# Kernel optimization log

Hardware: AMD Instinct MI355X
Metric: run time of the kernel (lower is better)

The kernel has to match this reference:

```python
import jax, jax.numpy as jnp
import numpy as np

H = 128   # d_model / features
N = 32    # kept complex modes (d_state=64 -> 32 conjugate pairs)
B = 8
L = 8192


def setup_inputs() -> dict:
    key = jax.random.key(0)
    ks = jax.random.split(key, 8)
    x = jax.random.normal(ks[0], (B, H, L), jnp.float32)
    # S4D (diagonal SSM) kernel parameters; channels=2 for bidirectional
    C_re = (jax.random.normal(ks[1], (2, H, N), jnp.float32) * (0.5 ** 0.5))
    C_im = (jax.random.normal(ks[2], (2, H, N), jnp.float32) * (0.5 ** 0.5))
    log_A_real = jnp.log(0.5 * jnp.ones((H, N), jnp.float32))          # S4D-Lin init
    A_imag = jnp.tile(np.pi * jnp.arange(N, dtype=jnp.float32), (H, 1))
    # log_dt uniform in [log(1e-3), log(1e-1)]
    u = jax.random.uniform(ks[3], (H,), jnp.float32)
    log_dt = u * (np.log(0.1) - np.log(0.001)) + np.log(0.001)
    D = jax.random.normal(ks[4], (H,), jnp.float32)                    # skip term
    W_pw = jax.random.normal(ks[5], (H, H), jnp.float32) / np.sqrt(H)  # 1x1 conv weight (out, in)
    gamma = jnp.ones((H,), jnp.float32)
    beta = jnp.zeros((H,), jnp.float32)
    return {"x": x, "C_re": C_re, "C_im": C_im, "log_A_real": log_A_real,
            "A_imag": A_imag, "log_dt": log_dt, "D": D, "W_pw": W_pw,
            "gamma": gamma, "beta": beta}


def reference(x, C_re, C_im, log_A_real, A_imag, log_dt, D, W_pw, gamma, beta):
    Lx = x.shape[-1]
    # ---- S4D SSM kernel via Vandermonde (ZOH discretization) ----
    A = -jnp.exp(log_A_real) + 1j * A_imag                 # (H, N) complex
    dt = jnp.exp(log_dt)[:, None]                          # (H, 1)
    dtA = A * dt                                           # (H, N)
    C = C_re + 1j * C_im                                   # (2, H, N)
    Kc = C * ((jnp.exp(dtA) - 1.0) / A)                    # (2, H, N)
    vand = jnp.exp(dtA[:, :, None] * jnp.arange(Lx))       # (H, N, L)
    k = 2.0 * jnp.einsum('chn,hnl->chl', Kc, vand).real    # (2, H, L)
    # ---- bidirectional: causal half + anticausal (flipped) half ----
    k_full = (jnp.pad(k[0], ((0, 0), (0, Lx)))
              + jnp.pad(k[1][:, ::-1], ((0, 0), (Lx, 0))))  # (H, 2L)
    # ---- FFT convolution ----
    n = 2 * Lx
    y = jnp.fft.irfft(jnp.fft.rfft(x, n=n) * jnp.fft.rfft(k_full, n=n), n=n)[..., :Lx]
    y = y + x * D[:, None]                                 # skip connection
    y = jax.nn.gelu(y, approximate=False)                  # FFTConv default activation
    # ---- pointwise 1x1 conv (no bias) ----
    y = jnp.einsum('bhl,oh->bol', y, W_pw)
    # ---- BatchNorm1d (training-mode batch statistics) ----
    mean = jnp.mean(y, axis=(0, 2), keepdims=True)
    var = jnp.var(y, axis=(0, 2), keepdims=True)
    y = (y - mean) * jax.lax.rsqrt(var + 1e-5) * gamma[:, None] + beta[:, None]
    # ---- ELU + residual (dropout p=0) ----
    return jax.nn.elu(y) + x
```

## Files before the change

kernel.cpp:

```cpp
#include <hip/hip_runtime.h>
#include <math.h>

#define HCH   128
#define NMODE 32
#define BB    8
#define LLEN  8192
#define LC    256
#define CCH   (LLEN / LC)
#define ROWS  (BB * HCH)

typedef unsigned int uint;
typedef _Float16 f16x8 __attribute__((ext_vector_type(8)));
typedef float    f32x4 __attribute__((ext_vector_type(4)));

static __device__ __forceinline__ uint pk2(float a, float b) {
    union { _Float16 h[2]; uint u; } v;
    v.h[0] = (_Float16)a; v.h[1] = (_Float16)b;
    return v.u;
}

__device__ __forceinline__ float gelu_f(float y) {
    float z = fabsf(y) * 0.7071067811865476f;
    float p = fmaf(z, 0.078108f, 0.000972f);
    p = fmaf(z, p, 0.230389f);
    p = fmaf(z, p, 0.278393f);
    p = fmaf(z, p, 1.0f);
    float p2 = p * p;
    float p4 = p2 * p2;
    float er = 1.f - __builtin_amdgcn_rcpf(p4);
    float s  = copysignf(er, y);
    return 0.5f * y * (1.f + s);
}

#define DPP_ADD(v, ctrl) { int _t = __builtin_amdgcn_update_dpp(0, __float_as_int(v), \
                             (ctrl), 0xF, 0xF, true); (v) += __int_as_float(_t); }

__global__ __launch_bounds__(256) void k_prep(const float* __restrict__ C_re,
                                              const float* __restrict__ C_im,
                                              const float* __restrict__ logA,
                                              const float* __restrict__ Aim,
                                              const float* __restrict__ logdt,
                                              const float* __restrict__ W,
                                              _Float16* __restrict__ cT,
                                              uint* __restrict__ kmg,
                                              _Float16* __restrict__ eT,
                                              _Float16* __restrict__ Wh,
                                              float* __restrict__ Pw,
                                              float* __restrict__ stats) {
    __shared__ float2 PL[32 * 257];
    __shared__ float4 G01[32];
    __shared__ float4 HG[32];
    __shared__ float2 WL[32];
    __shared__ float k0L[256], k1L[256];
    __shared__ _Float16 KMl[516];
    int tid  = threadIdx.x;
    int h    = blockIdx.x >> 1;
    int half = blockIdx.x & 1;
    if (blockIdx.x == 0) stats[tid] = 0.f;
    if (half == 0 && tid < 128) Wh[h * 128 + tid] = (_Float16)W[h * 128 + tid];
    if (tid < 32) {
        int n = tid, idx = h * 32 + n;
        float ar = expf(logA[idx]);
        float ai = Aim[idx];
        float dt = expf(logdt[h]);
        float dre = -ar * dt, dim = ai * dt;
        float er = expf(dre);
        float wr = er * cosf(dim), wi = er * sinf(dim);
        WL[n] = (float2){wr, wi};
        if (half == 0) {
            float eL = expf(dre * 256.f);
            Pw[idx]        = eL * cosf(dim * 256.f);
            Pw[4096 + idx] = eL * sinf(dim * 256.f);
        }
        float den  = ar * ar + ai * ai;
        float numr = -(wr - 1.f) * ar + wi * ai;
        float numi = -wi * ar - (wr - 1.f) * ai;
        float Kr = numr / den, Ki = numi / den;
        float c0r = C_re[idx],        c0i = C_im[idx];
        float c1r = C_re[4096 + idx], c1i = C_im[4096 + idx];
        float g0r = 2.f * (c0r * Kr - c0i * Ki), g0i = 2.f * (c0r * Ki + c0i * Kr);
        float g1r = 2.f * (c1r * Kr - c1i * Ki);
        float g1i = 2.f * (c1r * Ki + c1i * Kr);
        G01[n] = (float4){g0r, g0i, g1r, g1i};
        HG[n]  = (float4){g0r * wr - g0i * wi, g0r * wi + g0i * wr, g1r, g1i};
    }
    __syncthreads();
    {
        int n = tid & 31, tg = tid >> 5;
        float2 w = WL[n];
        float w2r = w.x * w.x - w.y * w.y,   w2i = 2.f * w.x * w.y;
        float w4r = w2r * w2r - w2i * w2i,   w4i = 2.f * w2r * w2i;
        float w8r = w4r * w4r - w4i * w4i,   w8i = 2.f * w4r * w4i;
        float pr = (tg & 1) ? w.x : 1.f;
        float pi = (tg & 1) ? w.y : 0.f;
        if (tg & 2) { float t2 = pr * w2r - pi * w2i; pi = pr * w2i + pi * w2r; pr = t2; }
        if (tg & 4) { float t4 = pr * w4r - pi * w4i; pi = pr * w4i + pi * w4r; pr = t4; }
        float2* row = &PL[n * 257];
        #pragma unroll
        for (int j = 0; j < 32; j++) {
            row[tg + 8 * j] = (float2){pr, pi};
            float tr = pr * w8r - pi * w8i; pi = pr * w8i + pi * w8r; pr = tr;
        }
    }
    __syncthreads();
    {
        int tau = tid;
        float s0 = 0.f, s1 = 0.f;
        #pragma unroll
        for (int n = 0; n < 32; n++) {
            float2 p = PL[n * 257 + tau];
            float4 g = G01[n];
            s0 += g.x * p.x - g.y * p.y;
            s1 += g.z * p.x - g.w * p.y;
        }
        k0L[tau] = s0; k1L[tau] = s1;
    }
    __syncthreads();
    if (half == 0) {
        KMl[tid]       = (_Float16)k0L[255 - tid];
        KMl[256 + tid] = (_Float16)k1L[tid];
        if (tid == 0) { KMl[512] = (_Float16)0.f; KMl[513] = (_Float16)0.f; }
    }
    __syncthreads();
    if (half == 0) {
        union { _Float16 hh[2]; uint u; } pa, pb;
        pa.hh[0] = KMl[2 * tid];     pa.hh[1] = KMl[2 * tid + 1];
        pb.hh[0] = KMl[2 * tid + 1]; pb.hh[1] = KMl[2 * tid + 2];
        kmg[(size_t)h * 512 + tid]       = pa.u;
        kmg[(size_t)h * 512 + 256 + tid] = pb.u;
    }
    #pragma unroll 4
    for (int i = 0; i < 16; i++) {
        int idx = i * 256 + tid;
        int n = idx & 31;
        int t = half * 128 + (idx >> 5);
        float2 pt = PL[n * 257 + t];
        float2 pu = PL[n * 257 + 255 - t];
        float4 hg = HG[n];
        size_t rb = ((size_t)(h * 256 + t)) * 128;
        *(uint*)&cT[rb + 2 * n]      = pk2(hg.x * pt.x - hg.y * pt.y,
                                           -(hg.x * pt.y + hg.y * pt.x));
        *(uint*)&cT[rb + 64 + 2 * n] = pk2(hg.z * pu.x - hg.w * pu.y,
                                           -(hg.z * pu.y + hg.w * pu.x));
    }
    #pragma unroll 4
    for (int i = 0; i < 16; i++) {
        int idx = i * 256 + tid;
        int n = idx >> 7;
        int s = half * 128 + (idx & 127);
        float2 ps = PL[n * 257 + s];
        float2 pu = PL[n * 257 + 255 - s];
        size_t base = (size_t)h * 128 * 256;
        eT[base + (size_t)(2 * n) * 256 + s]      = (_Float16)pu.x;
        eT[base + (size_t)(2 * n + 1) * 256 + s]  = (_Float16)pu.y;
        eT[base + (size_t)(64 + 2 * n) * 256 + s] = (_Float16)ps.x;
        eT[base + (size_t)(65 + 2 * n) * 256 + s] = (_Float16)ps.y;
    }
}

__global__ __launch_bounds__(256, 2) void k_states_c(const float* __restrict__ x,
                                                     const _Float16* __restrict__ eT,
                                                     const float* __restrict__ Pw,
                                                     _Float16* __restrict__ xh,
                                                     _Float16* __restrict__ carr) {
    __shared__ float Sf[128 * 66];
    _Float16* SMh = (_Float16*)Sf;
    int tid = threadIdx.x;
    int xcd = blockIdx.x & 7, slot = blockIdx.x >> 3;
    int h = xcd * 16 + (slot >> 2);
    int mt = (slot >> 1) & 1, d = slot & 1;
    int wave = tid >> 6, lane = tid & 63;
    int wm = wave >> 1, wn = wave & 1;
    int lrow = lane & 15, quad = lane >> 4;
    int koff = quad * 8;
    f32x4 acc[4][2];
    #pragma unroll
    for (int a = 0; a < 4; a++)
        #pragma unroll
        for (int b = 0; b < 2; b++) acc[a][b] = (f32x4){0.f, 0.f, 0.f, 0.f};

    const int chA = tid >> 3, segA = tid & 7;
    const size_t xbase = (((size_t)(mt * 4) * HCH + h) << 13) + (chA << 8) + segA * 4;
    const int rB = tid >> 2, sgB = tid & 3;

    float4 ar[4]; uint4 br;
    #define LOADA_S(kk) { _Pragma("unroll") for (int i = 0; i < 4; i++) \
        ar[i] = *(const float4*)(x + xbase + ((size_t)i << 20) + (kk)); }
    #define LOADB_S(kk) { br = *(const uint4*)(eT + ((size_t)(h * 128 + d * 64 + rB)) * 256 + (kk) + sgB * 8); }
    #define WRITE_S(buf, kk) { _Pragma("unroll") for (int i = 0; i < 4; i++) { \
            uint2 o; o.x = pk2(ar[i].x, ar[i].y); o.y = pk2(ar[i].z, ar[i].w); \
            *(uint2*)&SMh[(buf) * 5120 + (chA + 32 * i) * 40 + segA * 4] = o; \
            if (d == 0) *(uint2*)&xh[xbase + ((size_t)i << 20) + (kk)] = o; } \
        *(uint4*)&SMh[10240 + (buf) * 2560 + rB * 40 + sgB * 8] = br; }

    LOADA_S(0); LOADB_S(0);
    WRITE_S(0, 0);
    __syncthreads();
    for (int kt = 0; kt < 8; kt++) {
        int cur = kt & 1;
        if (kt < 7) { LOADA_S((kt + 1) * 32); LOADB_S((kt + 1) * 32); }
        f16x8 a[4], b[2];
        #pragma unroll
        for (int f = 0; f < 4; f++)
            a[f] = *(const f16x8*)&SMh[cur * 5120 + (wm * 64 + f * 16 + lrow) * 40 + koff];
        #pragma unroll
        for (int f = 0; f < 2; f++)
            b[f] = *(const f16x8*)&SMh[10240 + cur * 2560 + (wn * 32 + f * 16 + lrow) * 40 + koff];
        #pragma unroll
        for (int fi = 0; fi < 4; fi++)
            #pragma unroll
            for (int fj = 0; fj < 2; fj++)
                acc[fi][fj] = __builtin_amdgcn_mfma_f32_16x16x32_f16(a[fi], b[fj], acc[fi][fj], 0, 0, 0);
        if (kt < 7) {
            WRITE_S(cur ^ 1, (kt + 1) * 32);
            __syncthreads();
        }
    }
    __syncthreads();
    #pragma unroll
    for (int fi = 0; fi < 4; fi++) {
        #pragma unroll
        for (int fj = 0; fj < 2; fj++) {
            int srow = wn * 32 + fj * 16 + lrow;
            #pragma unroll
            for (int rg = 0; rg < 4; rg++) {
                int bc = wm * 64 + fi * 16 + quad * 4 + rg;
                Sf[bc * 66 + srow] = acc[fi][fj][rg];
            }
        }
    }
    __syncthreads();
    if (tid < 128) {
        int bloc = tid >> 5, n = tid & 31;
        float wLr = Pw[h * 32 + n], wLi = Pw[4096 + h * 32 + n];
        float cr = 0.f, ci = 0.f;
        size_t gb = ((size_t)(h * 256 + mt * 128 + bloc * 32)) * 128 + d * 64 + 2 * n;
        if (d == 0) {
            for (int c = 0; c < CCH; c++) {
                *(uint*)&carr[gb + (size_t)c * 128] = pk2(cr, ci);
                float2 s = *(const float2*)&Sf[(bloc * 32 + c) * 66 + 2 * n];
                float nr = fmaf(wLr, cr, -wLi * ci) + s.x;
                float ni = fmaf(wLi, cr,  wLr * ci) + s.y;
                cr = nr; ci = ni;
            }
        } else {
            for (int c = CCH - 1; c >= 0; c--) {
                *(uint*)&carr[gb + (size_t)c * 128] = pk2(cr, ci);
                float2 s = *(const float2*)&Sf[(bloc * 32 + c) * 66 + 2 * n];
                float nr = fmaf(wLr, cr, -wLi * ci) + s.x;
                float ni = fmaf(wLi, cr,  wLr * ci) + s.y;
                cr = nr; ci = ni;
            }
        }
    }
    #undef LOADA_S
    #undef LOADB_S
    #undef WRITE_S
}

__global__ __launch_bounds__(256, 2) void k_conv_g(const _Float16* __restrict__ xh,
                                                   const uint* __restrict__ kmg,
                                                   const _Float16* __restrict__ cT,
                                                   const _Float16* __restrict__ carr,
                                                   const float* __restrict__ D,
                                                   _Float16* __restrict__ Yg) {
    __shared__ _Float16 At[2][128 * 40];
    __shared__ _Float16 Bt[2][128 * 40];
    __shared__ uint KMA[256], KMB[256];
    int tid = threadIdx.x;
    int xcd = blockIdx.x & 7, slot = blockIdx.x >> 3;
    int p = xcd * 32 + (slot >> 1);
    int mt = slot & 1;
    int h = p >> 1, nt = p & 1;
    int wave = tid >> 6, lane = tid & 63;
    int wm = wave >> 1, wn = wave & 1;
    int lrow = lane & 15, quad = lane >> 4;
    int koff = quad * 8;
    f32x4 acc[4][4];
    #pragma unroll
    for (int a = 0; a < 4; a++)
        #pragma unroll
        for (int b = 0; b < 4; b++) acc[a][b] = (f32x4){0.f, 0.f, 0.f, 0.f};

    const int rS = tid >> 2, sgS = tid & 3;

    uint4 a_r[2], b_r[2];
    #define LOADA_C(kk) { _Pragma("unroll") for (int i = 0; i < 2; i++) { \
            int bc = mt * 128 + rS + 64 * i; \
            a_r[i] = ((kk) < 256) \
              ? *(const uint4*)(xh + (((size_t)((bc >> 5) * HCH + h)) << 13) + ((bc & 31) << 8) + (kk) + sgS * 8) \
              : *(const uint4*)(carr + ((size_t)(h * 256 + bc)) * 128 + ((kk) - 256) + sgS * 8); } }
    #define LOADB_C(kk) { _Pragma("unroll") for (int i = 0; i < 2; i++) \
        b_r[i] = *(const uint4*)(cT + ((size_t)(h * 256 + nt * 128 + rS + 64 * i)) * 128 + ((kk) - 256) + sgS * 8); }
    #define WRITE_A(buf) { _Pragma("unroll") for (int i = 0; i < 2; i++) \
        *(uint4*)&At[buf][(rS + 64 * i) * 40 + sgS * 8] = a_r[i]; }
    #define WRITE_B(buf) { _Pragma("unroll") for (int i = 0; i < 2; i++) \
        *(uint4*)&Bt[buf][(rS + 64 * i) * 40 + sgS * 8] = b_r[i]; }

    KMA[tid] = kmg[(size_t)h * 512 + tid];
    KMB[tid] = kmg[(size_t)h * 512 + 256 + tid];
    LOADA_C(0);
    WRITE_A(0);
    __syncthreads();
    for (int kt = 0; kt < 12; kt++) {
        int cur = kt & 1;
        if (kt < 11) {
            LOADA_C((kt + 1) * 32);
            if (kt + 1 >= 8) LOADB_C((kt + 1) * 32);
        }
        f16x8 a[4], b[4];
        #pragma unroll
        for (int f = 0; f < 4; f++)
            a[f] = *(const f16x8*)&At[cur][(wm * 64 + f * 16 + lrow) * 40 + koff];
        if (kt < 8) {
            int kk = kt * 32;
            #pragma unroll
            for (int f = 0; f < 4; f++) {
                int t_f = nt * 128 + wn * 64 + f * 16 + lrow;
                int idx0 = 255 - t_f + kk + koff;
                int par = idx0 & 1;
                int dw = idx0 >> 1;
                const uint* kp = par ? KMB : KMA;
                union { uint u[4]; f16x8 v; } bu;
                bu.u[0] = kp[dw]; bu.u[1] = kp[dw + 1]; bu.u[2] = kp[dw + 2]; bu.u[3] = kp[dw + 3];
                b[f] = bu.v;
            }
        } else {
            #pragma unroll
            for (int f = 0; f < 4; f++)
                b[f] = *(const f16x8*)&Bt[cur][(wn * 64 + f * 16 + lrow) * 40 + koff];
        }
        #pragma unroll
        for (int fi = 0; fi < 4; fi++)
            #pragma unroll
            for (int fj = 0; fj < 4; fj++)
                acc[fi][fj] = __builtin_amdgcn_mfma_f32_16x16x32_f16(a[fi], b[fj], acc[fi][fj], 0, 0, 0);
        if (kt < 11) {
            WRITE_A(cur ^ 1);
            if (kt + 1 >= 8) WRITE_B(cur ^ 1);
            __syncthreads();
        }
    }
    float Dh = D[h];
    #pragma unroll
    for (int fi = 0; fi < 4; fi++) {
        #pragma unroll
        for (int fj = 0; fj < 4; fj++) {
            int t = nt * 128 + wn * 64 + fj * 16 + lrow;
            #pragma unroll
            for (int rg = 0; rg < 4; rg++) {
                int bc = mt * 128 + wm * 64 + fi * 16 + quad * 4 + rg;
                size_t base = (((size_t)((bc >> 5) * HCH + h)) << 13) + ((bc & 31) << 8) + t;
                float xv = (float)xh[base];
                float yv = acc[fi][fj][rg] + Dh * xv;
                Yg[base] = (_Float16)gelu_f(yv);
            }
        }
    }
    #undef LOADA_C
    #undef LOADB_C
    #undef WRITE_A
    #undef WRITE_B
}

__global__ __launch_bounds__(256, 2) void k_pointwise(const _Float16* __restrict__ Yg,
                                                      const _Float16* __restrict__ Wh,
                                                      _Float16* __restrict__ z,
                                                      float* __restrict__ stats) {
    __shared__ _Float16 Yt[2][128 * 40];
    __shared__ float Ls[512];
    int tid = threadIdx.x;
    int b  = blockIdx.x >> 6;
    int l0 = (blockIdx.x & 63) << 7;
    int wave = tid >> 6, lane = tid & 63;
    int wm = wave >> 1, wn = wave & 1;
    int lrow = lane & 15, quad = lane >> 4;
    int koff = quad * 8;
    f32x4 acc[4][4];
    #pragma unroll
    for (int a = 0; a < 4; a++)
        #pragma unroll
        for (int c = 0; c < 4; c++) acc[a][c] = (f32x4){0.f, 0.f, 0.f, 0.f};

    f16x8 a[4][4];
    #pragma unroll
    for (int ks = 0; ks < 4; ks++)
        #pragma unroll
        for (int f = 0; f < 4; f++)
            a[ks][f] = *(const f16x8*)(Wh + (wm * 64 + f * 16 + lrow) * HCH + ks * 32 + koff);

    const int hhS = tid & 31;
    const int lgbase = tid >> 5;
    uint4 yv[2];
    #define LOADY(kk) { _Pragma("unroll") for (int i = 0; i < 2; i++) \
        yv[i] = *(const uint4*)(Yg + (((size_t)(b * HCH + (kk) + hhS)) << 13) + l0 + (lgbase + 8 * i) * 8); }
    #define WRITEY(buf) { _Pragma("unroll") for (int i = 0; i < 2; i++) { \
            const _Float16* hv = (const _Float16*)&yv[i]; \
            _Pragma("unroll") for (int j = 0; j < 8; j++) \
                Yt[buf][((lgbase + 8 * i) * 8 + j) * 40 + hhS] = hv[j]; } }

    LOADY(0);
    WRITEY(0);
    __syncthreads();
    for (int kt = 0; kt < 4; kt++) {
        int cur = kt & 1;
        if (kt < 3) LOADY((kt + 1) * 32);
        f16x8 bf[4];
        #pragma unroll
        for (int f = 0; f < 4; f++)
            bf[f] = *(const f16x8*)&Yt[cur][(wn * 64 + f * 16 + lrow) * 40 + koff];
        #pragma unroll
        for (int fi = 0; fi < 4; fi++)
            #pragma unroll
            for (int fj = 0; fj < 4; fj++)
                acc[fi][fj] = __builtin_amdgcn_mfma_f32_16x16x32_f16(a[kt][fi], bf[fj], acc[fi][fj], 0, 0, 0);
        if (kt < 3) {
            WRITEY(cur ^ 1);
            __syncthreads();
        }
    }
    #pragma unroll
    for (int fi = 0; fi < 4; fi++) {
        #pragma unroll
        for (int fj = 0; fj < 4; fj++) {
            int l = l0 + wn * 64 + fj * 16 + lrow;
            #pragma unroll
            for (int rg = 0; rg < 4; rg++) {
                int o = wm * 64 + fi * 16 + quad * 4 + rg;
                z[(((size_t)(b * HCH + o)) << 13) + l] = (_Float16)acc[fi][fj][rg];
            }
        }
    }
    #pragma unroll
    for (int fi = 0; fi < 4; fi++) {
        #pragma unroll
        for (int rg = 0; rg < 4; rg++) {
            float s = 0.f, q = 0.f;
            #pragma unroll
            for (int fj = 0; fj < 4; fj++) {
                float v = acc[fi][fj][rg];
                s += v; q = fmaf(v, v, q);
            }
            DPP_ADD(s, 0xB1); DPP_ADD(s, 0x4E); DPP_ADD(s, 0x141); DPP_ADD(s, 0x140);
            DPP_ADD(q, 0xB1); DPP_ADD(q, 0x4E); DPP_ADD(q, 0x141); DPP_ADD(q, 0x140);
            if (lrow == 0) {
                int olo = fi * 16 + quad * 4 + rg;
                Ls[wave * 64 + olo]       = s;
                Ls[256 + wave * 64 + olo] = q;
            }
        }
    }
    __syncthreads();
    if (tid < HCH) {
        int wmn = tid >> 6;
        int olo = tid & 63;
        float s = Ls[(wmn * 2) * 64 + olo] + Ls[(wmn * 2 + 1) * 64 + olo];
        float q = Ls[256 + (wmn * 2) * 64 + olo] + Ls[256 + (wmn * 2 + 1) * 64 + olo];
        atomicAdd(&stats[tid], s);
        atomicAdd(&stats[HCH + tid], q);
    }
    #undef LOADY
    #undef WRITEY
}

__global__ __launch_bounds__(256) void k_final(const _Float16* __restrict__ z,
                                               const float* __restrict__ x,
                                               const float* __restrict__ stats,
                                               const float* __restrict__ gamma,
                                               const float* __restrict__ beta,
                                               float* __restrict__ out) {
    size_t i8 = (size_t)blockIdx.x * 256 + threadIdx.x;
    int o = (int)((i8 >> 10) & (HCH - 1));
    const float inv_cnt = 1.f / (float)(BB * LLEN);
    float m   = stats[o] * inv_cnt;
    float var = stats[HCH + o] * inv_cnt - m * m;
    float rs  = rsqrtf(var + 1e-5f);
    float ga  = gamma[o] * rs;
    float bt  = beta[o] - m * ga;
    uint4 zv = ((const uint4*)z)[i8];
    const _Float16* zh = (const _Float16*)&zv;
    float4 xa = ((const float4*)x)[2 * i8];
    float4 xb = ((const float4*)x)[2 * i8 + 1];
    float4 ra, rb;
    { float t = fmaf((float)zh[0], ga, bt); float e = t > 0.f ? t : (__expf(t) - 1.f); ra.x = e + xa.x; }
    { float t = fmaf((float)zh[1], ga, bt); float e = t > 0.f ? t : (__expf(t) - 1.f); ra.y = e + xa.y; }
    { float t = fmaf((float)zh[2], ga, bt); float e = t > 0.f ? t : (__expf(t) - 1.f); ra.z = e + xa.z; }
    { float t = fmaf((float)zh[3], ga, bt); float e = t > 0.f ? t : (__expf(t) - 1.f); ra.w = e + xa.w; }
    { float t = fmaf((float)zh[4], ga, bt); float e = t > 0.f ? t : (__expf(t) - 1.f); rb.x = e + xb.x; }
    { float t = fmaf((float)zh[5], ga, bt); float e = t > 0.f ? t : (__expf(t) - 1.f); rb.y = e + xb.y; }
    { float t = fmaf((float)zh[6], ga, bt); float e = t > 0.f ? t : (__expf(t) - 1.f); rb.z = e + xb.z; }
    { float t = fmaf((float)zh[7], ga, bt); float e = t > 0.f ? t : (__expf(t) - 1.f); rb.w = e + xb.w; }
    ((float4*)out)[2 * i8]     = ra;
    ((float4*)out)[2 * i8 + 1] = rb;
}

extern "C" void kernel_launch(void* const* d_in, const int* in_sizes, int n_in,
                              void* d_out, int out_size, void* d_ws, size_t ws_size,
                              hipStream_t stream) {
    const float* x     = (const float*)d_in[0];
    const float* C_re  = (const float*)d_in[1];
    const float* C_im  = (const float*)d_in[2];
    const float* logA  = (const float*)d_in[3];
    const float* Aim   = (const float*)d_in[4];
    const float* logdt = (const float*)d_in[5];
    const float* D     = (const float*)d_in[6];
    const float* W     = (const float*)d_in[7];
    const float* gamma = (const float*)d_in[8];
    const float* beta  = (const float*)d_in[9];

    float* ws = (float*)d_ws;
    _Float16* eT    = (_Float16*)ws;
    _Float16* Yg    = (_Float16*)ws;
    _Float16* zf    = (_Float16*)(ws + 8388608);
    _Float16* cT    = (_Float16*)(ws + 12582912);
    uint*     kmg   = (uint*)(ws + 14680064);
    _Float16* carr  = (_Float16*)(ws + 16777216);
    float*    Pw    = ws + 16777216 + 2097152;
    float*    stats = Pw + 8192;
    _Float16* Wh    = (_Float16*)(ws + 18882880);
    _Float16* xh    = (_Float16*)(ws + 18891072);
    float*    out   = (float*)d_out;

    k_prep     <<<256,  256, 0, stream>>>(C_re, C_im, logA, Aim, logdt, W, cT, kmg, eT, Wh, Pw, stats);
    k_states_c <<<512,  256, 0, stream>>>(x, eT, Pw, xh, carr);
    k_conv_g   <<<512,  256, 0, stream>>>(xh, kmg, cT, carr, D, Yg);
    k_pointwise<<<512,  256, 0, stream>>>(Yg, Wh, zf, stats);
    k_final    <<<4096, 256, 0, stream>>>(zf, x, stats, gamma, beta, out);
}
```

Before: 178.4 us.

## Merge prep and chunk-state kernels into one role-split launch, compute powers on-chip

Replaces the separate prep and chunk-state kernels with one launch whose blocks take one of two roles. One role builds the SSM kernel tables, the other computes chunk states. The state blocks now generate the decay-power matrix directly in LDS instead of reading the eT table from global memory, and they recompute the chunk-length power instead of reading Pw. This removes a kernel launch boundary and the eT write/read round trip. The costs are redundant transcendental math per block, a serial power loop, and a larger LDS footprint that may lower occupancy.

```diff
diff --git a/kernel.cpp b/kernel.cpp
--- a/kernel.cpp
+++ b/kernel.cpp
@@ -35,144 +35,171 @@
 #define DPP_ADD(v, ctrl) { int _t = __builtin_amdgcn_update_dpp(0, __float_as_int(v), \
                              (ctrl), 0xF, 0xF, true); (v) += __int_as_float(_t); }
 
-__global__ __launch_bounds__(256) void k_prep(const float* __restrict__ C_re,
-                                              const float* __restrict__ C_im,
-                                              const float* __restrict__ logA,
-                                              const float* __restrict__ Aim,
-                                              const float* __restrict__ logdt,
-                                              const float* __restrict__ W,
-                                              _Float16* __restrict__ cT,
-                                              uint* __restrict__ kmg,
-                                              _Float16* __restrict__ eT,
-                                              _Float16* __restrict__ Wh,
-                                              float* __restrict__ Pw,
-                                              float* __restrict__ stats) {
-    __shared__ float2 PL[32 * 257];
-    __shared__ float4 G01[32];
-    __shared__ float4 HG[32];
-    __shared__ float2 WL[32];
-    __shared__ float k0L[256], k1L[256];
-    __shared__ _Float16 KMl[516];
-    int tid  = threadIdx.x;
-    int h    = blockIdx.x >> 1;
-    int half = blockIdx.x & 1;
-    if (blockIdx.x == 0) stats[tid] = 0.f;
-    if (half == 0 && tid < 128) Wh[h * 128 + tid] = (_Float16)W[h * 128 + tid];
-    if (tid < 32) {
-        int n = tid, idx = h * 32 + n;
-        float ar = expf(logA[idx]);
-        float ai = Aim[idx];
-        float dt = expf(logdt[h]);
-        float dre = -ar * dt, dim = ai * dt;
-        float er = expf(dre);
-        float wr = er * cosf(dim), wi = er * sinf(dim);
-        WL[n] = (float2){wr, wi};
+__global__ __launch_bounds__(256, 2) void k_front(const float* __restrict__ x,
+                                                  const float* __restrict__ C_re,
+                                                  const float* __restrict__ C_im,
+                                                  const float* __restrict__ logA,
+                                                  const float* __restrict__ Aim,
+                                                  const float* __restrict__ logdt,
+                                                  const float* __restrict__ W,
+                                                  _Float16* __restrict__ cT,
+                                                  uint* __restrict__ kmg,
+                                                  _Float16* __restrict__ Wh,
+                                                  float* __restrict__ stats,
+                                                  _Float16* __restrict__ xh,
+                                                  _Float16* __restrict__ carr) {
+    __shared__ float4 SMEM[4400];
+    int tid = threadIdx.x;
+    int role = blockIdx.x % 3;
+
+    if (role == 2) {
+        int pidx = blockIdx.x / 3;
+        int h    = pidx >> 1;
+        int half = pidx & 1;
+        char* base = (char*)SMEM;
+        float2*   PL  = (float2*)base;
+        float4*   G01 = (float4*)(base + 65792);
+        float4*   HG  = (float4*)(base + 66304);
+        float2*   WL  = (float2*)(base + 66816);
+        float*    k0L = (float*) (base + 67072);
+        float*    k1L = (float*) (base + 68096);
+        _Float16* KMl = (_Float16*)(base + 69120);
+
+        if (pidx == 0) stats[tid] = 0.f;
+        if (half == 0 && tid < 128) Wh[h * 128 + tid] = (_Float16)W[h * 128 + tid];
+        if (tid < 32) {
+            int n = tid, idx = h * 32 + n;
+            float ar = expf(logA[idx]);
+            float ai = Aim[idx];
+            float dt = expf(logdt[h]);
+            float dre = -ar * dt, dim = ai * dt;
+            float er = expf(dre);
+            float wr = er * cosf(dim), wi = er * sinf(dim);
+            WL[n] = (float2){wr, wi};
+            float den  = ar * ar + ai * ai;
+            float numr = -(wr - 1.f) * ar + wi * ai;
+            float numi = -wi * ar - (wr - 1.f) * ai;
+            float Kr = numr / den, Ki = numi / den;
+            float c0r = C_re[idx],        c0i = C_im[idx];
+            float c1r = C_re[4096 + idx], c1i = C_im[4096 + idx];
+            float g0r = 2.f * (c0r * Kr - c0i * Ki), g0i = 2.f * (c0r * Ki + c0i * Kr);
+            float g1r = 2.f * (c1r * Kr - c1i * Ki);
+            float g1i = 2.f * (c1r * Ki + c1i * Kr);
+            G01[n] = (float4){g0r, g0i, g1r, g1i};
+            HG[n]  = (float4){g0r * wr - g0i * wi, g0r * wi + g0i * wr, g1r, g1i};
+        }
+        __syncthreads();
+        {
+            int n = tid & 31, tg = tid >> 5;
+            float2 w = WL[n];
+            float w2r = w.x * w.x - w.y * w.y,   w2i = 2.f * w.x * w.y;
+            float w4r = w2r * w2r - w2i * w2i,   w4i = 2.f * w2r * w2i;
+            float w8r = w4r * w4r - w4i * w4i,   w8i = 2.f * w4r * w4i;
+            float pr = (tg & 1) ? w.x : 1.f;
+            float pi = (tg & 1) ? w.y : 0.f;
+            if (tg & 2) { float t2 = pr * w2r - pi * w2i; pi = pr * w2i + pi * w2r; pr = t2; }
+            if (tg & 4) { float t4 = pr * w4r - pi * w4i; pi = pr * w4i + pi * w4r; pr = t4; }
+            float2* row = &PL[n * 257];
+            #pragma unroll
+            for (int j = 0; j < 32; j++) {
+                row[tg + 8 * j] = (float2){pr, pi};
+                float tr = pr * w8r - pi * w8i; pi = pr * w8i + pi * w8r; pr = tr;
+            }
+        }
+        __syncthreads();
+        {
+            int tau = tid;
+            float s0 = 0.f, s1 = 0.f;
+            #pragma unroll
+            for (int n = 0; n < 32; n++) {
+                float2 p = PL[n * 257 + tau];
+                float4 g = G01[n];
+                s0 += g.x * p.x - g.y * p.y;
+                s1 += g.z * p.x - g.w * p.y;
+            }
+            k0L[tau] = s0; k1L[tau] = s1;
+        }
+        __syncthreads();
         if (half == 0) {
-            float eL = expf(dre * 256.f);
-            Pw[idx]        = eL * cosf(dim * 256.f);
-            Pw[4096 + idx] = eL * sinf(dim * 256.f);
-        }
-        float den  = ar * ar + ai * ai;
-        float numr = -(wr - 1.f) * ar + wi * ai;
-        float numi = -wi * ar - (wr - 1.f) * ai;
-        float Kr = numr / den, Ki = numi / den;
-        float c0r = C_re[idx],        c0i = C_im[idx];
-        float c1r = C_re[4096 + idx], c1i = C_im[4096 + idx];
-        float g0r = 2.f * (c0r * Kr - c0i * Ki), g0i = 2.f * (c0r * Ki + c0i * Kr);
-        float g1r = 2.f * (c1r * Kr - c1i * Ki);
-        float g1i = 2.f * (c1r * Ki + c1i * Kr);
-        G01[n] = (float4){g0r, g0i, g1r, g1i};
-        HG[n]  = (float4){g0r * wr - g0i * wi, g0r * wi + g0i * wr, g1r, g1i};
-    }
-    __syncthreads();
-    {
-        int n = tid & 31, tg = tid >> 5;
-        float2 w = WL[n];
-        float w2r = w.x * w.x - w.y * w.y,   w2i = 2.f * w.x * w.y;
-        float w4r = w2r * w2r - w2i * w2i,   w4i = 2.f * w2r * w2i;
-        float w8r = w4r * w4r - w4i * w4i,   w8i = 2.f * w4r * w4i;
-        float pr = (tg & 1) ? w.x : 1.f;
-        float pi = (tg & 1) ? w.y : 0.f;
-        if (tg & 2) { float t2 = pr * w2r - pi * w2i; pi = pr * w2i + pi * w2r; pr = t2; }
-        if (tg & 4) { float t4 = pr * w4r - pi * w4i; pi = pr * w4i + pi * w4r; pr = t4; }
-        float2* row = &PL[n * 257];
-        #pragma unroll
-        for (int j = 0; j < 32; j++) {
-            row[tg + 8 * j] = (float2){pr, pi};
-            float tr = pr * w8r - pi * w8i; pi = pr * w8i + pi * w8r; pr = tr;
-        }
-    }
-    __syncthreads();
-    {
-        int tau = tid;
-        float s0 = 0.f, s1 = 0.f;
-        #pragma unroll
-        for (int n = 0; n < 32; n++) {
-            float2 p = PL[n * 257 + tau];
-            float4 g = G01[n];
-            s0 += g.x * p.x - g.y * p.y;
-            s1 += g.z * p.x - g.w * p.y;
-        }
-        k0L[tau] = s0; k1L[tau] = s1;
-    }
-    __syncthreads();
-    if (half == 0) {
-        KMl[tid]       = (_Float16)k0L[255 - tid];
-        KMl[256 + tid] = (_Float16)k1L[tid];
-        if (tid == 0) { KMl[512] = (_Float16)0.f; KMl[513] = (_Float16)0.f; }
-    }
-    __syncthreads();
-    if (half == 0) {
-        union { _Float16 hh[2]; uint u; } pa, pb;
-        pa.hh[0] = KMl[2 * tid];     pa.hh[1] = KMl[2 * tid + 1];
-        pb.hh[0] = KMl[2 * tid + 1]; pb.hh[1] = KMl[2 * tid + 2];
-        kmg[(size_t)h * 512 + tid]       = pa.u;
-        kmg[(size_t)h * 512 + 256 + tid] = pb.u;
-    }
-    #pragma unroll 4
-    for (int i = 0; i < 16; i++) {
-        int idx = i * 256 + tid;
-        int n = idx & 31;
-        int t = half * 128 + (idx >> 5);
-        float2 pt = PL[n * 257 + t];
-        float2 pu = PL[n * 257 + 255 - t];
-        float4 hg = HG[n];
-        size_t rb = ((size_t)(h * 256 + t)) * 128;
-        *(uint*)&cT[rb + 2 * n]      = pk2(hg.x * pt.x - hg.y * pt.y,
-                                           -(hg.x * pt.y + hg.y * pt.x));
-        *(uint*)&cT[rb + 64 + 2 * n] = pk2(hg.z * pu.x - hg.w * pu.y,
-                                           -(hg.z * pu.y + hg.w * pu.x));
-    }
-    #pragma unroll 4
-    for (int i = 0; i < 16; i++) {
-        int idx = i * 256 + tid;
-        int n = idx >> 7;
-        int s = half * 128 + (idx & 127);
-        float2 ps = PL[n * 257 + s];
-        float2 pu = PL[n * 257 + 255 - s];
-        size_t base = (size_t)h * 128 * 256;
-        eT[base + (size_t)(2 * n) * 256 + s]      = (_Float16)pu.x;
-        eT[base + (size_t)(2 * n + 1) * 256 + s]  = (_Float16)pu.y;
-        eT[base + (size_t)(64 + 2 * n) * 256 + s] = (_Float16)ps.x;
-        eT[base + (size_t)(65 + 2 * n) * 256 + s] = (_Float16)ps.y;
-    }
-}
-
-__global__ __launch_bounds__(256, 2) void k_states_c(const float* __restrict__ x,
-                                                     const _Float16* __restrict__ eT,
-                                                     const float* __restrict__ Pw,
-                                                     _Float16* __restrict__ xh,
-                                                     _Float16* __restrict__ carr) {
-    __shared__ float Sf[128 * 66];
-    _Float16* SMh = (_Float16*)Sf;
-    int tid = threadIdx.x;
-    int xcd = blockIdx.x & 7, slot = blockIdx.x >> 3;
+            KMl[tid]       = (_Float16)k0L[255 - tid];
+            KMl[256 + tid] = (_Float16)k1L[tid];
+            if (tid == 0) { KMl[512] = (_Float16)0.f; KMl[513] = (_Float16)0.f; }
+        }
+        __syncthreads();
+        if (half == 0) {
+            union { _Float16 hh[2]; uint u; } pa, pb;
+            pa.hh[0] = KMl[2 * tid];     pa.hh[1] = KMl[2 * tid + 1];
+            pb.hh[0] = KMl[2 * tid + 1]; pb.hh[1] = KMl[2 * tid + 2];
+            kmg[(size_t)h * 512 + tid]       = pa.u;
+            kmg[(size_t)h * 512 + 256 + tid] = pb.u;
+        }
+        #pragma unroll 4
+        for (int i = 0; i < 16; i++) {
+            int idx = i * 256 + tid;
+            int n = idx & 31;
+            int t = half * 128 + (idx >> 5);
+            float2 pt = PL[n * 257 + t];
+            float2 pu = PL[n * 257 + 255 - t];
+            float4 hg = HG[n];
+            size_t rb = ((size_t)(h * 256 + t)) * 128;
+            *(uint*)&cT[rb + 2 * n]      = pk2(hg.x * pt.x - hg.y * pt.y,
+                                               -(hg.x * pt.y + hg.y * pt.x));
+            *(uint*)&cT[rb + 64 + 2 * n] = pk2(hg.z * pu.x - hg.w * pu.y,
+                                               -(hg.z * pu.y + hg.w * pu.x));
+        }
+        return;
+    }
+
+    int sidx = (blockIdx.x / 3) * 2 + role;
+    int xcd = sidx & 7, slot = sidx >> 3;
     int h = xcd * 16 + (slot >> 2);
     int mt = (slot >> 1) & 1, d = slot & 1;
+
+    char* base = (char*)SMEM;
+    _Float16* Bloc = (_Float16*)base;
+    _Float16* At   = (_Float16*)(base + 34048);
+    float*    Sf   = (float*)base;
+
     int wave = tid >> 6, lane = tid & 63;
     int wm = wave >> 1, wn = wave & 1;
     int lrow = lane & 15, quad = lane >> 4;
     int koff = quad * 8;
+
+    {
+        int r = tid >> 2, q = tid & 3;
+        int n = r >> 1, c = r & 1;
+        int idxp = h * 32 + n;
+        float ar = expf(logA[idxp]), ai = Aim[idxp];
+        float dtv = expf(logdt[h]);
+        float dre = -ar * dtv, dim = ai * dtv;
+        float er = expf(dre);
+        float wr = er * cosf(dim), wi = er * sinf(dim);
+        float br = wr, bi = wi;
+        #pragma unroll
+        for (int k = 0; k < 6; k++) { float t2 = br * br - bi * bi; bi = 2.f * br * bi; br = t2; }
+        int m64 = d ? q : (3 - q);
+        float pr = 1.f, pi = 0.f;
+        for (int k = 0; k < m64; k++) { float t2 = pr * br - pi * bi; pi = pr * bi + pi * br; pr = t2; }
+        int s0 = q * 64;
+        if (d == 0) {
+            #pragma unroll 8
+            for (int m = 31; m >= 0; m--) {
+                float hr = pr, hi2 = pi;
+                float t2 = pr * wr - pi * wi; pi = pr * wi + pi * wr; pr = t2;
+                *(uint*)&Bloc[r * 266 + s0 + 2 * m] = pk2(c ? pi : pr, c ? hi2 : hr);
+                t2 = pr * wr - pi * wi; pi = pr * wi + pi * wr; pr = t2;
+            }
+        } else {
+            #pragma unroll 8
+            for (int m = 0; m < 32; m++) {
+                float lr = pr, li = pi;
+                float t2 = pr * wr - pi * wi; pi = pr * wi + pi * wr; pr = t2;
+                *(uint*)&Bloc[r * 266 + s0 + 2 * m] = pk2(c ? li : lr, c ? pi : pr);
+                t2 = pr * wr - pi * wi; pi = pr * wi + pi * wr; pr = t2;
+            }
+        }
+    }
+
     f32x4 acc[4][2];
     #pragma unroll
     for (int a = 0; a < 4; a++)
@@ -181,31 +208,28 @@
 
     const int chA = tid >> 3, segA = tid & 7;
     const size_t xbase = (((size_t)(mt * 4) * HCH + h) << 13) + (chA << 8) + segA * 4;
-    const int rB = tid >> 2, sgB = tid & 3;
-
-    float4 ar[4]; uint4 br;
+
+    float4 ar4[4];
     #define LOADA_S(kk) { _Pragma("unroll") for (int i = 0; i < 4; i++) \
-        ar[i] = *(const float4*)(x + xbase + ((size_t)i << 20) + (kk)); }
-    #define LOADB_S(kk) { br = *(const uint4*)(eT + ((size_t)(h * 128 + d * 64 + rB)) * 256 + (kk) + sgB * 8); }
+        ar4[i] = *(const float4*)(x + xbase + ((size_t)i << 20) + (kk)); }
     #define WRITE_S(buf, kk) { _Pragma("unroll") for (int i = 0; i < 4; i++) { \
-            uint2 o; o.x = pk2(ar[i].x, ar[i].y); o.y = pk2(ar[i].z, ar[i].w); \
-            *(uint2*)&SMh[(buf) * 5120 + (chA + 32 * i) * 40 + segA * 4] = o; \
-            if (d == 0) *(uint2*)&xh[xbase + ((size_t)i << 20) + (kk)] = o; } \
-        *(uint4*)&SMh[10240 + (buf) * 2560 + rB * 40 + sgB * 8] = br; }
-
-    LOADA_S(0); LOADB_S(0);
+            uint2 o; o.x = pk2(ar4[i].x, ar4[i].y); o.y = pk2(ar4[i].z, ar4[i].w); \
+            *(uint2*)&At[(buf) * 5120 + (chA + 32 * i) * 40 + segA * 4] = o; \
+            if (d == 0) *(uint2*)&xh[xbase + ((size_t)i << 20) + (kk)] = o; } }
+
+    LOADA_S(0);
     WRITE_S(0, 0);
     __syncthreads();
     for (int kt = 0; kt < 8; kt++) {
         int cur = kt & 1;
-        if (kt < 7) { LOADA_S((kt + 1) * 32); LOADB_S((kt + 1) * 32); }
+        if (kt < 7) LOADA_S((kt + 1) * 32);
         f16x8 a[4], b[2];
         #pragma unroll
         for (int f = 0; f < 4; f++)
-            a[f] = *(const f16x8*)&SMh[cur * 5120 + (wm * 64 + f * 16 + lrow) * 40 + koff];
+            a[f] = *(const f16x8*)&At[cur * 5120 + (wm * 64 + f * 16 + lrow) * 40 + koff];
         #pragma unroll
         for (int f = 0; f < 2; f++)
-            b[f] = *(const f16x8*)&SMh[10240 + cur * 2560 + (wn * 32 + f * 16 + lrow) * 40 + koff];
+            b[f] = *(const f16x8*)&Bloc[(wn * 32 + f * 16 + lrow) * 266 + kt * 32 + koff];
         #pragma unroll
         for (int fi = 0; fi < 4; fi++)
             #pragma unroll
@@ -232,7 +256,12 @@
     __syncthreads();
     if (tid < 128) {
         int bloc = tid >> 5, n = tid & 31;
-        float wLr = Pw[h * 32 + n], wLi = Pw[4096 + h * 32 + n];
+        int idxp = h * 32 + n;
+        float arp = expf(logA[idxp]), aip = Aim[idxp];
+        float dtv = expf(logdt[h]);
+        float eL = expf(-arp * dtv * 256.f);
+        float ang = aip * dtv * 256.f;
+        float wLr = eL * cosf(ang), wLi = eL * sinf(ang);
         float cr = 0.f, ci = 0.f;
         size_t gb = ((size_t)(h * 256 + mt * 128 + bloc * 32)) * 128 + d * 64 + 2 * n;
         if (d == 0) {
@@ -254,7 +283,6 @@
         }
     }
     #undef LOADA_S
-    #undef LOADB_S
     #undef WRITE_S
 }
 
@@ -509,20 +537,17 @@
     const float* beta  = (const float*)d_in[9];
 
     float* ws = (float*)d_ws;
-    _Float16* eT    = (_Float16*)ws;
     _Float16* Yg    = (_Float16*)ws;
     _Float16* zf    = (_Float16*)(ws + 8388608);
     _Float16* cT    = (_Float16*)(ws + 12582912);
     uint*     kmg   = (uint*)(ws + 14680064);
     _Float16* carr  = (_Float16*)(ws + 16777216);
-    float*    Pw    = ws + 16777216 + 2097152;
-    float*    stats = Pw + 8192;
-    _Float16* Wh    = (_Float16*)(ws + 18882880);
-    _Float16* xh    = (_Float16*)(ws + 18891072);
+    float*    stats = ws + 16777216 + 2097152;
+    _Float16* Wh    = (_Float16*)(ws + 18874688);
+    _Float16* xh    = (_Float16*)(ws + 18882880);
     float*    out   = (float*)d_out;
 
-    k_prep     <<<256,  256, 0, stream>>>(C_re, C_im, logA, Aim, logdt, W, cT, kmg, eT, Wh, Pw, stats);
-    k_states_c <<<512,  256, 0, stream>>>(x, eT, Pw, xh, carr);
+    k_front    <<<768,  256, 0, stream>>>(x, C_re, C_im, logA, Aim, logdt, W, cT, kmg, Wh, stats, xh, carr);
     k_conv_g   <<<512,  256, 0, stream>>>(xh, kmg, cT, carr, D, Yg);
     k_pointwise<<<512,  256, 0, stream>>>(Yg, Wh, zf, stats);
     k_final    <<<4096, 256, 0, stream>>>(zf, x, stats, gamma, beta, out);
```

Measured after the change: 190.5 us. 6.8% more time.

## Shrink conv tile to 128x64 and preload swizzled C-matrix tile into LDS

Applied to the files above, without the earlier changes.

The chunked-conv GEMM kernel now uses a 128x64 output tile instead of 128x128, doubling the grid to 1024 blocks and raising launch bounds to 4 blocks per CU. The cT operand for the state-contribution phase is loaded once up front into an XOR-swizzled LDS buffer, replacing its per-iteration double-buffered staging. This aims to raise occupancy and remove the B-operand streaming in the loop. In exchange, the xh/carr A-operand is reloaded by twice as many blocks, and each block does less MFMA work per loaded byte.

```diff
diff --git a/kernel.cpp b/kernel.cpp
--- a/kernel.cpp
+++ b/kernel.cpp
@@ -258,65 +258,65 @@
     #undef WRITE_S
 }
 
-__global__ __launch_bounds__(256, 2) void k_conv_g(const _Float16* __restrict__ xh,
+__global__ __launch_bounds__(256, 4) void k_conv_g(const _Float16* __restrict__ xh,
                                                    const uint* __restrict__ kmg,
                                                    const _Float16* __restrict__ cT,
                                                    const _Float16* __restrict__ carr,
                                                    const float* __restrict__ D,
                                                    _Float16* __restrict__ Yg) {
     __shared__ _Float16 At[2][128 * 40];
-    __shared__ _Float16 Bt[2][128 * 40];
+    __shared__ _Float16 Bc[64 * 128];
     __shared__ uint KMA[256], KMB[256];
     int tid = threadIdx.x;
     int xcd = blockIdx.x & 7, slot = blockIdx.x >> 3;
-    int p = xcd * 32 + (slot >> 1);
-    int mt = slot & 1;
-    int h = p >> 1, nt = p & 1;
+    int h   = xcd * 16 + (slot >> 3);
+    int sub = slot & 7;
+    int mt = sub >> 2, nt = sub & 3;
     int wave = tid >> 6, lane = tid & 63;
     int wm = wave >> 1, wn = wave & 1;
     int lrow = lane & 15, quad = lane >> 4;
     int koff = quad * 8;
-    f32x4 acc[4][4];
+    f32x4 acc[4][2];
     #pragma unroll
     for (int a = 0; a < 4; a++)
         #pragma unroll
-        for (int b = 0; b < 4; b++) acc[a][b] = (f32x4){0.f, 0.f, 0.f, 0.f};
+        for (int b = 0; b < 2; b++) acc[a][b] = (f32x4){0.f, 0.f, 0.f, 0.f};
 
     const int rS = tid >> 2, sgS = tid & 3;
 
-    uint4 a_r[2], b_r[2];
+    uint4 a_r[2];
     #define LOADA_C(kk) { _Pragma("unroll") for (int i = 0; i < 2; i++) { \
             int bc = mt * 128 + rS + 64 * i; \
             a_r[i] = ((kk) < 256) \
               ? *(const uint4*)(xh + (((size_t)((bc >> 5) * HCH + h)) << 13) + ((bc & 31) << 8) + (kk) + sgS * 8) \
               : *(const uint4*)(carr + ((size_t)(h * 256 + bc)) * 128 + ((kk) - 256) + sgS * 8); } }
-    #define LOADB_C(kk) { _Pragma("unroll") for (int i = 0; i < 2; i++) \
-        b_r[i] = *(const uint4*)(cT + ((size_t)(h * 256 + nt * 128 + rS + 64 * i)) * 128 + ((kk) - 256) + sgS * 8); }
     #define WRITE_A(buf) { _Pragma("unroll") for (int i = 0; i < 2; i++) \
         *(uint4*)&At[buf][(rS + 64 * i) * 40 + sgS * 8] = a_r[i]; }
-    #define WRITE_B(buf) { _Pragma("unroll") for (int i = 0; i < 2; i++) \
-        *(uint4*)&Bt[buf][(rS + 64 * i) * 40 + sgS * 8] = b_r[i]; }
 
     KMA[tid] = kmg[(size_t)h * 512 + tid];
     KMB[tid] = kmg[(size_t)h * 512 + 256 + tid];
+    #pragma unroll
+    for (int i = 0; i < 4; i++) {
+        int idx = tid + i * 256;
+        int r = idx >> 4, sg = idx & 15;
+        uint4 v = *(const uint4*)(cT + ((size_t)(h * 256 + nt * 64 + r)) * 128 + sg * 8);
+        *(uint4*)&Bc[r * 128 + ((sg * 8) ^ ((r & 7) << 3))] = v;
+    }
     LOADA_C(0);
     WRITE_A(0);
     __syncthreads();
     for (int kt = 0; kt < 12; kt++) {
         int cur = kt & 1;
-        if (kt < 11) {
-            LOADA_C((kt + 1) * 32);
-            if (kt + 1 >= 8) LOADB_C((kt + 1) * 32);
-        }
-        f16x8 a[4], b[4];
+        if (kt < 11) LOADA_C((kt + 1) * 32);
+        f16x8 a[4], b[2];
         #pragma unroll
         for (int f = 0; f < 4; f++)
             a[f] = *(const f16x8*)&At[cur][(wm * 64 + f * 16 + lrow) * 40 + koff];
         if (kt < 8) {
             int kk = kt * 32;
             #pragma unroll
-            for (int f = 0; f < 4; f++) {
-                int t_f = nt * 128 + wn * 64 + f * 16 + lrow;
+            for (int f = 0; f < 2; f++) {
+                int t_f = nt * 64 + wn * 32 + f * 16 + lrow;
                 int idx0 = 255 - t_f + kk + koff;
                 int par = idx0 & 1;
                 int dw = idx0 >> 1;
@@ -326,18 +326,20 @@
                 b[f] = bu.v;
             }
         } else {
-            #pragma unroll
-            for (int f = 0; f < 4; f++)
-                b[f] = *(const f16x8*)&Bt[cur][(wn * 64 + f * 16 + lrow) * 40 + koff];
+            int cb = kt * 32 - 256 + koff;
+            #pragma unroll
+            for (int f = 0; f < 2; f++) {
+                int r2 = wn * 32 + f * 16 + lrow;
+                b[f] = *(const f16x8*)&Bc[r2 * 128 + (cb ^ ((r2 & 7) << 3))];
+            }
         }
         #pragma unroll
         for (int fi = 0; fi < 4; fi++)
             #pragma unroll
-            for (int fj = 0; fj < 4; fj++)
+            for (int fj = 0; fj < 2; fj++)
                 acc[fi][fj] = __builtin_amdgcn_mfma_f32_16x16x32_f16(a[fi], b[fj], acc[fi][fj], 0, 0, 0);
         if (kt < 11) {
             WRITE_A(cur ^ 1);
-            if (kt + 1 >= 8) WRITE_B(cur ^ 1);
             __syncthreads();
         }
     }
@@ -345,8 +347,8 @@
     #pragma unroll
     for (int fi = 0; fi < 4; fi++) {
         #pragma unroll
-        for (int fj = 0; fj < 4; fj++) {
-            int t = nt * 128 + wn * 64 + fj * 16 + lrow;
+        for (int fj = 0; fj < 2; fj++) {
+            int t = nt * 64 + wn * 32 + fj * 16 + lrow;
             #pragma unroll
             for (int rg = 0; rg < 4; rg++) {
                 int bc = mt * 128 + wm * 64 + fi * 16 + quad * 4 + rg;
@@ -358,9 +360,7 @@
         }
     }
     #undef LOADA_C
-    #undef LOADB_C
     #undef WRITE_A
-    #undef WRITE_B
 }
 
 __global__ __launch_bounds__(256, 2) void k_pointwise(const _Float16* __restrict__ Yg,
@@ -523,7 +523,7 @@
 
     k_prep     <<<256,  256, 0, stream>>>(C_re, C_im, logA, Aim, logdt, W, cT, kmg, eT, Wh, Pw, stats);
     k_states_c <<<512,  256, 0, stream>>>(x, eT, Pw, xh, carr);
-    k_conv_g   <<<512,  256, 0, stream>>>(xh, kmg, cT, carr, D, Yg);
+    k_conv_g   <<<1024, 256, 0, stream>>>(xh, kmg, cT, carr, D, Yg);
     k_pointwise<<<512,  256, 0, stream>>>(Yg, Wh, zf, stats);
     k_final    <<<4096, 256, 0, stream>>>(zf, x, stats, gamma, beta, out);
 }
```

After: 174.0 us. -2.5%, faster.
